# Performance work log

Measured on AMD Instinct MI355X. Metric: run time of the kernel, lower is better.

The kernel has to match this reference:

```python
import jax, jax.numpy as jnp
import numpy as np

N = 8192        # number of nodes (dense adjacency)
IN_DIM = 128    # GCN in_dim
OUT_DIM = 128   # GCN out_dim
MASK_THRESH = 0.8
NEG_INF = 1e9


def setup_inputs() -> dict:
    key = jax.random.key(0)
    kA, kX, kW = jax.random.split(key, 3)
    A = jax.random.uniform(kA, (N, N), dtype=jnp.float32)
    X = jax.random.normal(kX, (N, IN_DIM), dtype=jnp.float32)
    # nn.Linear(in_dim, out_dim): weight [out_dim, in_dim], bias [out_dim]
    W = jax.random.normal(kW, (OUT_DIM, IN_DIM), dtype=jnp.float32) * (1.0 / np.sqrt(IN_DIM))
    b = jnp.zeros((OUT_DIM,), dtype=jnp.float32)
    return {"A": A, "X": X, "W": W, "b": b}


def reference(A, X, W, b):
    # GCN.forward: A_norm = softmax(A - 1e9 * (A <= 0.8), axis=-1)
    # out = leaky_relu(A_norm @ Linear(X))   (relu=True path)
    logits = A - NEG_INF * (A <= MASK_THRESH).astype(A.dtype)   # [N, N]
    A_norm = jax.nn.softmax(logits, axis=-1)                     # row-wise softmax
    XW = X @ W.T + b                                             # [N, OUT_DIM]
    return jax.nn.leaky_relu(A_norm @ XW, negative_slope=0.01)   # [N, OUT_DIM]
```

## Files before the change

kernel.cpp:

```cpp
#include <hip/hip_runtime.h>
#include <hip/hip_bf16.h>

#define N_NODES 8192
#define DIM 128
#define MASK_THRESH 0.8f
#define ROWS 64
#define RB (N_NODES / ROWS)
#define KSTEP 64

using f32x4  = __attribute__((ext_vector_type(4))) float;
using bf16x8 = __attribute__((ext_vector_type(8))) short;

static __device__ __forceinline__ short f2bf(float f) {
    unsigned u = __builtin_bit_cast(unsigned, f);
    u += 0x7fffu + ((u >> 16) & 1u);
    return (short)(u >> 16);
}

static __device__ __forceinline__ void gload16(const void* gsrc, void* ldst) {
    __builtin_amdgcn_global_load_lds(
        (const __attribute__((address_space(1))) unsigned int*)gsrc,
        (__attribute__((address_space(3))) unsigned int*)ldst,
        16, 0, 0);
}

__global__ __launch_bounds__(256) void build_vf_kernel(
    const float* __restrict__ X, const float* __restrict__ W,
    const float* __restrict__ bias, short* __restrict__ Vf) {
    __shared__ float xs[32][128];
    const int jt = blockIdx.x * 32;
    for (int e = threadIdx.x; e < 32 * 128; e += 256) {
        xs[e >> 7][e & 127] = X[(size_t)(jt + (e >> 7)) * DIM + (e & 127)];
    }
    __syncthreads();
    const int d  = threadIdx.x & 127;
    const int jh = threadIdx.x >> 7;
    float bv = bias[d];
    float acc[16];
#pragma unroll
    for (int i = 0; i < 16; i++) acc[i] = bv;
    const float* wrow = W + (size_t)d * DIM;
    for (int k = 0; k < DIM; k += 4) {
        f32x4 wv = *(const f32x4*)(wrow + k);
#pragma unroll
        for (int i = 0; i < 16; i++) {
            f32x4 xv = *(const f32x4*)(&xs[jh * 16 + i][k]);
            acc[i] = fmaf(xv[0], wv[0], acc[i]);
            acc[i] = fmaf(xv[1], wv[1], acc[i]);
            acc[i] = fmaf(xv[2], wv[2], acc[i]);
            acc[i] = fmaf(xv[3], wv[3], acc[i]);
        }
    }
    bf16x8 o0, o1;
#pragma unroll
    for (int i = 0; i < 8; i++) { o0[i] = f2bf(acc[i]); o1[i] = f2bf(acc[8 + i]); }
    const int kb = jt >> 5;
    const int t  = d >> 4;
    short* base = Vf + ((size_t)(kb * 8 + t) * 64 + (d & 15) + 32 * jh) * 8;
    *(bf16x8*)(base)       = o0;
    *(bf16x8*)(base + 128) = o1;
}

template <int WRITE_PARTIAL>
__global__ __launch_bounds__(512, 4) void fused_kernel(
    const float* __restrict__ A, const short* __restrict__ Vf,
    float* __restrict__ dst, float* __restrict__ Zp, int kchunk, int S) {

    __shared__ __align__(16) float abuf[2 * 64 * 64];
    __shared__ __align__(16) short vbuf[2 * 16 * 512];
    __shared__ float zs[64];

    const int tid   = threadIdx.x;
    const int wid   = tid >> 6;
    const int lane  = tid & 63;
    const int row_a = lane & 15;
    const int kg    = lane >> 4;
    const int wr    = wid >> 2;
    const int wc    = wid & 3;
    const int rb    = blockIdx.x / S;
    const int chunk = blockIdx.x - rb * S;
    const int r0    = rb * ROWS;
    const int k0    = chunk * kchunk;
    const int nsteps = kchunk >> 6;

    const float* asrcA[2]; int adstA[2];
#pragma unroll
    for (int i = 0; i < 2; i++) {
        const int rowt = wid * 8 + i * 4 + (lane >> 4);
        asrcA[i] = A + (size_t)(r0 + rowt) * N_NODES + k0
                     + (((lane & 15) ^ (rowt & 15)) << 2);
        adstA[i] = (wid * 8 + i * 4) * 64;
    }
    const short* vsrcV = Vf + ((size_t)(k0 >> 5) * 8 + wid * 2) * 512 + lane * 8;
    const int vdst0 = wid * 2 * 512;

    f32x4 acc[2][2];
#pragma unroll
    for (int rg = 0; rg < 2; rg++)
#pragma unroll
        for (int t = 0; t < 2; t++) acc[rg][t] = (f32x4)0.0f;
    float zacc[2] = {0.0f, 0.0f};

    auto stage = [&](int s, int b) {
#pragma unroll
        for (int i = 0; i < 2; i++)
            gload16(asrcA[i] + (size_t)s * KSTEP, abuf + b * 4096 + adstA[i]);
#pragma unroll
        for (int j = 0; j < 2; j++)
            gload16(vsrcV + (size_t)s * 8192 + j * 512, vbuf + b * 8192 + vdst0 + j * 512);
    };

    stage(0, 0);
    stage(1, 1);

    for (int ks = 0; ks < nsteps; ks++) {
        asm volatile("s_waitcnt vmcnt(4)\n\ts_barrier" ::: "memory");

        const float* ab = abuf + (ks & 1) * 4096;
        const short* vb = vbuf + (ks & 1) * 8192;
#pragma unroll
        for (int kb = 0; kb < 2; kb++) {
            const bf16x8 bv0 = *(const bf16x8*)(vb + (kb * 8 + wc * 2 + 0) * 512 + lane * 8);
            const bf16x8 bv1 = *(const bf16x8*)(vb + (kb * 8 + wc * 2 + 1) * 512 + lane * 8);
#pragma unroll
            for (int rg = 0; rg < 2; rg++) {
                const int rbase = (wr * 32 + rg * 16 + row_a) * 64;
                const int c0    = kb * 8 + kg * 2;
                const f32x4 av0 = *(const f32x4*)(ab + rbase + (((c0 + 0) ^ row_a) << 2));
                const f32x4 av1 = *(const f32x4*)(ab + rbase + (((c0 + 1) ^ row_a) << 2));
                float p[8];
#pragma unroll
                for (int i = 0; i < 4; i++) {
                    p[i]     = (av0[i] > MASK_THRESH) ? __expf(av0[i]) : 0.0f;
                    p[i + 4] = (av1[i] > MASK_THRESH) ? __expf(av1[i]) : 0.0f;
                }
                bf16x8 af;
#pragma unroll
                for (int i = 0; i < 8; i++) { zacc[rg] += p[i]; af[i] = f2bf(p[i]); }
                acc[rg][0] = __builtin_amdgcn_mfma_f32_16x16x32_bf16(af, bv0, acc[rg][0], 0, 0, 0);
                acc[rg][1] = __builtin_amdgcn_mfma_f32_16x16x32_bf16(af, bv1, acc[rg][1], 0, 0, 0);
            }
        }

        asm volatile("s_barrier" ::: "memory");
        const int stg = (ks + 2 < nsteps) ? (ks + 2) : (nsteps - 1);
        stage(stg, ks & 1);
    }

    asm volatile("s_waitcnt vmcnt(0)" ::: "memory");
    __syncthreads();

#pragma unroll
    for (int rg = 0; rg < 2; rg++) {
        zacc[rg] += __shfl_xor(zacc[rg], 16);
        zacc[rg] += __shfl_xor(zacc[rg], 32);
    }

    if (WRITE_PARTIAL) {
        float* nd = dst + (size_t)chunk * N_NODES * DIM;
#pragma unroll
        for (int rg = 0; rg < 2; rg++)
#pragma unroll
            for (int t = 0; t < 2; t++)
#pragma unroll
                for (int r = 0; r < 4; r++) {
                    const int row = r0 + wr * 32 + rg * 16 + kg * 4 + r;
                    const int col = wc * 32 + t * 16 + row_a;
                    nd[(size_t)row * DIM + col] = acc[rg][t][r];
                }
        if (wc == 0 && lane < 16) {
#pragma unroll
            for (int rg = 0; rg < 2; rg++)
                Zp[(size_t)chunk * N_NODES + r0 + wr * 32 + rg * 16 + lane] = zacc[rg];
        }
    } else {
        if (wc == 0 && lane < 16) {
#pragma unroll
            for (int rg = 0; rg < 2; rg++) zs[wr * 32 + rg * 16 + lane] = zacc[rg];
        }
        __syncthreads();
#pragma unroll
        for (int rg = 0; rg < 2; rg++)
#pragma unroll
            for (int t = 0; t < 2; t++)
#pragma unroll
                for (int r = 0; r < 4; r++) {
                    const int rl  = wr * 32 + rg * 16 + kg * 4 + r;
                    const int col = wc * 32 + t * 16 + row_a;
                    const float v = acc[rg][t][r] / zs[rl];
                    dst[(size_t)(r0 + rl) * DIM + col] = (v > 0.0f) ? v : 0.01f * v;
                }
    }
}

__global__ __launch_bounds__(256) void reduce_kernel(
    const float* __restrict__ num, const float* __restrict__ Zp,
    float* __restrict__ out, int S) {
    const size_t i4 = (size_t)blockIdx.x * 256 + threadIdx.x;
    const int r  = (int)(i4 >> 5);
    const int c4 = (int)(i4 & 31) * 4;
    f32x4 s = (f32x4)0.0f;
    float z = 0.0f;
    for (int p = 0; p < S; p++) {
        s += *(const f32x4*)(num + ((size_t)p * N_NODES + r) * DIM + c4);
        z += Zp[(size_t)p * N_NODES + r];
    }
    f32x4 o;
#pragma unroll
    for (int j = 0; j < 4; j++) {
        const float v = s[j] / z;
        o[j] = (v > 0.0f) ? v : 0.01f * v;
    }
    *(f32x4*)(out + (size_t)r * DIM + c4) = o;
}

extern "C" void kernel_launch(void* const* d_in, const int* in_sizes, int n_in,
                              void* d_out, int out_size, void* d_ws, size_t ws_size,
                              hipStream_t stream) {
    const float* A = (const float*)d_in[0];
    const float* X = (const float*)d_in[1];
    const float* W = (const float*)d_in[2];
    const float* b = (const float*)d_in[3];
    float* out = (float*)d_out;

    const size_t VF_BYTES = (size_t)DIM * N_NODES * 2;
    short* Vf = (short*)d_ws;
    build_vf_kernel<<<N_NODES / 32, 256, 0, stream>>>(X, W, b, Vf);

    const size_t per_split = ((size_t)N_NODES * DIM + N_NODES) * sizeof(float);
    int S = 1;
    for (int cand = 4; cand >= 1; cand >>= 1) {
        if (VF_BYTES + (size_t)cand * per_split <= ws_size) { S = cand; break; }
    }

    if (S >= 2) {
        float* num = (float*)((char*)d_ws + VF_BYTES);
        float* Zp  = num + (size_t)S * N_NODES * DIM;
        fused_kernel<1><<<RB * S, 512, 0, stream>>>(A, Vf, num, Zp, N_NODES / S, S);
        reduce_kernel<<<(N_NODES * DIM / 4) / 256, 256, 0, stream>>>(num, Zp, out, S);
    } else {
        fused_kernel<0><<<RB, 512, 0, stream>>>(A, Vf, out, nullptr, N_NODES, 1);
    }
}
```

Before: 109.3 us.

## Shrink row tile to 32 with 4-wave blocks and raise split-K to 8

```diff
diff --git a/kernel.cpp b/kernel.cpp
--- a/kernel.cpp
+++ b/kernel.cpp
@@ -4,7 +4,7 @@
 #define N_NODES 8192
 #define DIM 128
 #define MASK_THRESH 0.8f
-#define ROWS 64
+#define ROWS 32
 #define RB (N_NODES / ROWS)
 #define KSTEP 64
 
@@ -62,21 +62,21 @@
 }
 
 template <int WRITE_PARTIAL>
-__global__ __launch_bounds__(512, 4) void fused_kernel(
+__global__ __launch_bounds__(256, 3) void fused_kernel(
     const float* __restrict__ A, const short* __restrict__ Vf,
     float* __restrict__ dst, float* __restrict__ Zp, int kchunk, int S) {
 
-    __shared__ __align__(16) float abuf[2 * 64 * 64];
-    __shared__ __align__(16) short vbuf[2 * 16 * 512];
-    __shared__ float zs[64];
+    __shared__ __align__(16) float smem_a[2 * 32 * 64];
+    __shared__ __align__(16) short smem_v[2 * 16 * 512];
+    __shared__ float zs2[2][16];
 
     const int tid   = threadIdx.x;
     const int wid   = tid >> 6;
     const int lane  = tid & 63;
     const int row_a = lane & 15;
     const int kg    = lane >> 4;
-    const int wr    = wid >> 2;
-    const int wc    = wid & 3;
+    const int wr    = wid >> 1;
+    const int wc    = wid & 1;
     const int rb    = blockIdx.x / S;
     const int chunk = blockIdx.x - rb * S;
     const int r0    = rb * ROWS;
@@ -91,105 +91,85 @@
                      + (((lane & 15) ^ (rowt & 15)) << 2);
         adstA[i] = (wid * 8 + i * 4) * 64;
     }
-    const short* vsrcV = Vf + ((size_t)(k0 >> 5) * 8 + wid * 2) * 512 + lane * 8;
-    const int vdst0 = wid * 2 * 512;
-
-    f32x4 acc[2][2];
-#pragma unroll
-    for (int rg = 0; rg < 2; rg++)
-#pragma unroll
-        for (int t = 0; t < 2; t++) acc[rg][t] = (f32x4)0.0f;
-    float zacc[2] = {0.0f, 0.0f};
+    const short* vsrcV = Vf + ((size_t)(k0 >> 5) * 8 + wid * 4) * 512 + lane * 8;
+    const int vdst0 = wid * 4 * 512;
+
+    f32x4 acc[4];
+#pragma unroll
+    for (int t = 0; t < 4; t++) acc[t] = (f32x4)0.0f;
+    float zacc = 0.0f;
 
     auto stage = [&](int s, int b) {
 #pragma unroll
         for (int i = 0; i < 2; i++)
-            gload16(asrcA[i] + (size_t)s * KSTEP, abuf + b * 4096 + adstA[i]);
-#pragma unroll
-        for (int j = 0; j < 2; j++)
-            gload16(vsrcV + (size_t)s * 8192 + j * 512, vbuf + b * 8192 + vdst0 + j * 512);
+            gload16(asrcA[i] + (size_t)s * KSTEP, smem_a + b * 2048 + adstA[i]);
+#pragma unroll
+        for (int j = 0; j < 4; j++)
+            gload16(vsrcV + (size_t)s * 8192 + j * 512, smem_v + b * 8192 + vdst0 + j * 512);
+    };
+
+    auto compute = [&](const float* ab, const short* vb) {
+        const int rL = wr * 16 + row_a;
+#pragma unroll
+        for (int kb = 0; kb < 2; kb++) {
+            const int c0 = kb * 8 + kg * 2;
+            const f32x4 av0 = *(const f32x4*)(ab + rL * 64 + (((c0 + 0) ^ row_a) << 2));
+            const f32x4 av1 = *(const f32x4*)(ab + rL * 64 + (((c0 + 1) ^ row_a) << 2));
+            float p[8];
+#pragma unroll
+            for (int i = 0; i < 4; i++) {
+                p[i]     = (av0[i] > MASK_THRESH) ? __expf(av0[i]) : 0.0f;
+                p[i + 4] = (av1[i] > MASK_THRESH) ? __expf(av1[i]) : 0.0f;
+            }
+            bf16x8 af;
+#pragma unroll
+            for (int i = 0; i < 8; i++) { zacc += p[i]; af[i] = f2bf(p[i]); }
+#pragma unroll
+            for (int t = 0; t < 4; t++) {
+                const bf16x8 bv = *(const bf16x8*)(vb + (kb * 8 + wc * 4 + t) * 512 + lane * 8);
+                acc[t] = __builtin_amdgcn_mfma_f32_16x16x32_bf16(af, bv, acc[t], 0, 0, 0);
+            }
+        }
     };
 
     stage(0, 0);
     stage(1, 1);
 
-    for (int ks = 0; ks < nsteps; ks++) {
-        asm volatile("s_waitcnt vmcnt(4)\n\ts_barrier" ::: "memory");
-
-        const float* ab = abuf + (ks & 1) * 4096;
-        const short* vb = vbuf + (ks & 1) * 8192;
-#pragma unroll
-        for (int kb = 0; kb < 2; kb++) {
-            const bf16x8 bv0 = *(const bf16x8*)(vb + (kb * 8 + wc * 2 + 0) * 512 + lane * 8);
-            const bf16x8 bv1 = *(const bf16x8*)(vb + (kb * 8 + wc * 2 + 1) * 512 + lane * 8);
-#pragma unroll
-            for (int rg = 0; rg < 2; rg++) {
-                const int rbase = (wr * 32 + rg * 16 + row_a) * 64;
-                const int c0    = kb * 8 + kg * 2;
-                const f32x4 av0 = *(const f32x4*)(ab + rbase + (((c0 + 0) ^ row_a) << 2));
-                const f32x4 av1 = *(const f32x4*)(ab + rbase + (((c0 + 1) ^ row_a) << 2));
-                float p[8];
-#pragma unroll
-                for (int i = 0; i < 4; i++) {
-                    p[i]     = (av0[i] > MASK_THRESH) ? __expf(av0[i]) : 0.0f;
-                    p[i + 4] = (av1[i] > MASK_THRESH) ? __expf(av1[i]) : 0.0f;
-                }
-                bf16x8 af;
-#pragma unroll
-                for (int i = 0; i < 8; i++) { zacc[rg] += p[i]; af[i] = f2bf(p[i]); }
-                acc[rg][0] = __builtin_amdgcn_mfma_f32_16x16x32_bf16(af, bv0, acc[rg][0], 0, 0, 0);
-                acc[rg][1] = __builtin_amdgcn_mfma_f32_16x16x32_bf16(af, bv1, acc[rg][1], 0, 0, 0);
-            }
-        }
-
+    for (int ks = 0; ks < nsteps - 1; ks++) {
+        asm volatile("s_waitcnt vmcnt(6)\n\ts_barrier" ::: "memory");
+        compute(smem_a + (ks & 1) * 2048, smem_v + (ks & 1) * 8192);
         asm volatile("s_barrier" ::: "memory");
-        const int stg = (ks + 2 < nsteps) ? (ks + 2) : (nsteps - 1);
-        stage(stg, ks & 1);
-    }
-
-    asm volatile("s_waitcnt vmcnt(0)" ::: "memory");
+        if (ks + 2 < nsteps) stage(ks + 2, ks & 1);
+    }
+    asm volatile("s_waitcnt vmcnt(0)\n\ts_barrier" ::: "memory");
+    compute(smem_a + ((nsteps - 1) & 1) * 2048, smem_v + ((nsteps - 1) & 1) * 8192);
+
+    zacc += __shfl_xor(zacc, 16);
+    zacc += __shfl_xor(zacc, 32);
+    if (wc == 0 && lane < 16) zs2[wr][lane] = zacc;
     __syncthreads();
 
-#pragma unroll
-    for (int rg = 0; rg < 2; rg++) {
-        zacc[rg] += __shfl_xor(zacc[rg], 16);
-        zacc[rg] += __shfl_xor(zacc[rg], 32);
-    }
-
     if (WRITE_PARTIAL) {
-        float* nd = dst + (size_t)chunk * N_NODES * DIM;
-#pragma unroll
-        for (int rg = 0; rg < 2; rg++)
-#pragma unroll
-            for (int t = 0; t < 2; t++)
-#pragma unroll
-                for (int r = 0; r < 4; r++) {
-                    const int row = r0 + wr * 32 + rg * 16 + kg * 4 + r;
-                    const int col = wc * 32 + t * 16 + row_a;
-                    nd[(size_t)row * DIM + col] = acc[rg][t][r];
-                }
-        if (wc == 0 && lane < 16) {
-#pragma unroll
-            for (int rg = 0; rg < 2; rg++)
-                Zp[(size_t)chunk * N_NODES + r0 + wr * 32 + rg * 16 + lane] = zacc[rg];
-        }
+#pragma unroll
+        for (int t = 0; t < 4; t++)
+#pragma unroll
+            for (int r = 0; r < 4; r++) {
+                const int rl  = wr * 16 + kg * 4 + r;
+                const int col = wc * 64 + t * 16 + row_a;
+                dst[((size_t)chunk * N_NODES + r0 + rl) * DIM + col] = acc[t][r];
+            }
+        if (wc == 0 && lane < 16)
+            Zp[(size_t)chunk * N_NODES + r0 + wr * 16 + lane] = zacc;
     } else {
-        if (wc == 0 && lane < 16) {
-#pragma unroll
-            for (int rg = 0; rg < 2; rg++) zs[wr * 32 + rg * 16 + lane] = zacc[rg];
-        }
-        __syncthreads();
-#pragma unroll
-        for (int rg = 0; rg < 2; rg++)
-#pragma unroll
-            for (int t = 0; t < 2; t++)
-#pragma unroll
-                for (int r = 0; r < 4; r++) {
-                    const int rl  = wr * 32 + rg * 16 + kg * 4 + r;
-                    const int col = wc * 32 + t * 16 + row_a;
-                    const float v = acc[rg][t][r] / zs[rl];
-                    dst[(size_t)(r0 + rl) * DIM + col] = (v > 0.0f) ? v : 0.01f * v;
-                }
+#pragma unroll
+        for (int t = 0; t < 4; t++)
+#pragma unroll
+            for (int r = 0; r < 4; r++) {
+                const int rl  = wr * 16 + kg * 4 + r;
+                const int col = wc * 64 + t * 16 + row_a;
+                const float v = acc[t][r] / zs2[wr][kg * 4 + r];
+                dst[(size_t)(r0 + rl) * DIM + col] = (v > 0.0f) ? v : 0.01f * v;
+            }
     }
 }
 
@@ -229,16 +209,16 @@
 
     const size_t per_split = ((size_t)N_NODES * DIM + N_NODES) * sizeof(float);
     int S = 1;
-    for (int cand = 4; cand >= 1; cand >>= 1) {
+    for (int cand = 8; cand >= 1; cand >>= 1) {
         if (VF_BYTES + (size_t)cand * per_split <= ws_size) { S = cand; break; }
     }
 
     if (S >= 2) {
         float* num = (float*)((char*)d_ws + VF_BYTES);
         float* Zp  = num + (size_t)S * N_NODES * DIM;
-        fused_kernel<1><<<RB * S, 512, 0, stream>>>(A, Vf, num, Zp, N_NODES / S, S);
+        fused_kernel<1><<<RB * S, 256, 0, stream>>>(A, Vf, num, Zp, N_NODES / S, S);
         reduce_kernel<<<(N_NODES * DIM / 4) / 256, 256, 0, stream>>>(num, Zp, out, S);
     } else {
-        fused_kernel<0><<<RB, 512, 0, stream>>>(A, Vf, out, nullptr, N_NODES, 1);
-    }
-}
+        fused_kernel<0><<<RB, 256, 0, stream>>>(A, Vf, out, nullptr, N_NODES, 1);
+    }
+}
```

Result: slower. 118.5 us (+8.4%).
